# Optimization experiments

Measured on AMD Instinct MI355X. Metric: run time of the kernel, lower is better.

The kernel has to match this reference:

```python
import jax, jax.numpy as jnp
import numpy as np

EMBED_DIM = 1024
NUM_HEADS = 16
HEAD_DIM = EMBED_DIM // NUM_HEADS
SCALE = HEAD_DIM ** -0.5


def setup_inputs() -> dict:
    key = jax.random.key(0)
    ks = jax.random.split(key, 11)
    b, n, c = 2, 2048, EMBED_DIM
    # xavier_uniform bound for square [c, c] weight
    bound = float(np.sqrt(6.0 / (c + c)))
    def xavier(k):
        return jax.random.uniform(k, (c, c), jnp.float32, -bound, bound)
    return {
        "q": jax.random.normal(ks[0], (b, n, c), jnp.float32),
        "k": jax.random.normal(ks[1], (b, n, c), jnp.float32),
        "v": jax.random.normal(ks[2], (b, n, c), jnp.float32),
        "wq": xavier(ks[3]), "bq": jnp.zeros((c,), jnp.float32),
        "wk": xavier(ks[4]), "bk": jnp.zeros((c,), jnp.float32),
        "wv": xavier(ks[5]), "bv": jnp.zeros((c,), jnp.float32),
        "wo": xavier(ks[6]), "bo": jnp.zeros((c,), jnp.float32),
    }


def reference(q, k, v, wq, bq, wk, bk, wv, bv, wo, bo):
    b, n, c = q.shape
    h, d = NUM_HEADS, HEAD_DIM
    # linear projections (torch Linear: x @ W^T + b)
    qh = (q @ wq.T + bq).reshape(b, n, h, d).transpose(0, 2, 1, 3)  # b h n d
    kh = (k @ wk.T + bk).reshape(b, n, h, d).transpose(0, 2, 1, 3)
    vh = (v @ wv.T + bv).reshape(b, n, h, d).transpose(0, 2, 1, 3)
    dots = jnp.einsum('bhid,bhjd->bhij', qh, kh) * SCALE
    attn = jax.nn.softmax(dots, axis=-1)  # dropout p=0 -> identity
    out = jnp.einsum('bhij,bhjd->bhid', attn, vh)
    out = out.transpose(0, 2, 1, 3).reshape(b, n, c)
    return out @ wo.T + bo
```

## Files before the change

kernel.cpp:

```cpp
#include <hip/hip_runtime.h>


typedef float f32x4 __attribute__((ext_vector_type(4)));
typedef float f32x16 __attribute__((ext_vector_type(16)));
typedef __bf16 bf16x8 __attribute__((ext_vector_type(8)));

#define SEQ 2048
#define CH 1024
#define NH 16
#define HD 64
#define TOK 4096
#define QSCALE 0.18033688011112042f

__device__ __forceinline__ unsigned short f2b(float f) {
  unsigned int u = __float_as_uint(f);
  u = (u + 0x7FFFu + ((u >> 16) & 1u)) >> 16;
  return (unsigned short)u;
}

__device__ __forceinline__ float fexp2(float x) {
  float r;
  asm("v_exp_f32 %0, %1" : "=v"(r) : "v"(x));
  return r;
}

__device__ __forceinline__ unsigned int cvtpk(float lo, float hi) {
  unsigned int r;
  asm("v_cvt_pk_bf16_f32 %0, %1, %2" : "=v"(r) : "v"(lo), "v"(hi));
  return r;
}

__device__ __forceinline__ void gload16(const void* g, void* l) {
  __builtin_amdgcn_global_load_lds(
      (const __attribute__((address_space(1))) unsigned int*)g,
      (__attribute__((address_space(3))) unsigned int*)l, 16, 0, 0);
}

struct CvtArgs {
  const float* src[4];
  unsigned short* dst[4];
  int n4[4];
};

__global__ __launch_bounds__(256) void cvt_kernel(CvtArgs a) {
  const int s = blockIdx.y;
  const int n4 = a.n4[s];
  const float4* __restrict__ src = (const float4*)a.src[s];
  unsigned short* __restrict__ dst = a.dst[s];
  const int stride = gridDim.x * blockDim.x;
  for (int i = blockIdx.x * blockDim.x + threadIdx.x; i < n4; i += stride) {
    float4 w = src[i];
    ushort4 o;
    o.x = f2b(w.x); o.y = f2b(w.y); o.z = f2b(w.z); o.w = f2b(w.w);
    *(ushort4*)(dst + 4 * (size_t)i) = o;
  }
}

struct Proj3Args {
  const float* X[3];
  const unsigned short* W[3];
  const float* bias[3];
  unsigned short* outb[3];
  int mode[3];
};

#define P3_ABYTES 16384
#define P3_BUFB (P3_ABYTES + 8192)

__device__ __forceinline__ void p3_stage(
    const float* __restrict__ X, const unsigned short* __restrict__ W,
    int mt, int nt, int k0, unsigned char* buf, int wid, int lane) {
#pragma unroll
  for (int is = 0; is < 4; ++is) {
    const int p = wid * 4096 + is * 1024 + lane * 16;
    const int row = p >> 7;
    const int so = ((p & 127) ^ ((row & 7) << 4)) >> 2;
    gload16(X + (size_t)(mt * 128 + row) * CH + k0 + so, buf + p);
  }
#pragma unroll
  for (int is = 0; is < 2; ++is) {
    const int p = wid * 2048 + is * 1024 + lane * 16;
    const int row = p >> 6;
    const int so = ((p & 63) ^ ((row & 3) << 4)) >> 1;
    gload16(W + (size_t)(nt * 128 + row) * CH + k0 + so, buf + P3_ABYTES + p);
  }
}

__global__ __launch_bounds__(256, 3) void proj3_kernel(Proj3Args a) {
  __shared__ __align__(16) unsigned char smem[2 * P3_BUFB];
  const int z = blockIdx.z;
  const float* __restrict__ X = a.X[z];
  const unsigned short* __restrict__ W = a.W[z];
  const float* __restrict__ bias = a.bias[z];
  unsigned short* __restrict__ outb = a.outb[z];
  const int mode = a.mode[z];
  const int tid = threadIdx.x, wid = tid >> 6, lane = tid & 63;
  const int wm = wid >> 1, wn = wid & 1;
  const int mt = blockIdx.x, nt = blockIdx.y;
  const int l15 = lane & 15, l4 = lane >> 4;

  float bvv[4];
#pragma unroll
  for (int nj = 0; nj < 4; ++nj)
    bvv[nj] = bias[nt * 128 + wn * 64 + nj * 16 + l15];

  f32x4 acc[4][4] = {};

  p3_stage(X, W, mt, nt, 0, smem, wid, lane);
  p3_stage(X, W, mt, nt, 32, smem + P3_BUFB, wid, lane);

  for (int s = 0; s < 32; ++s) {
    if (s < 31) asm volatile("s_waitcnt vmcnt(6)" ::: "memory");
    else        asm volatile("s_waitcnt vmcnt(0)" ::: "memory");
    __builtin_amdgcn_s_barrier();
    __builtin_amdgcn_sched_barrier(0);

    unsigned char* Al = smem + (s & 1) * P3_BUFB;
    unsigned char* Bl = Al + P3_ABYTES;

    bf16x8 af[4], bfr[4];
#pragma unroll
    for (int mi = 0; mi < 4; ++mi) {
      const int r = wm * 64 + mi * 16 + l15;
      const int swz = (r & 7) << 4;
      const f32x4 lo = *(const f32x4*)(Al + r * 128 + ((l4 * 32) ^ swz));
      const f32x4 hi = *(const f32x4*)(Al + r * 128 + ((l4 * 32 + 16) ^ swz));
      const uint4 aw = make_uint4(cvtpk(lo[0], lo[1]), cvtpk(lo[2], lo[3]),
                                  cvtpk(hi[0], hi[1]), cvtpk(hi[2], hi[3]));
      af[mi] = *(const bf16x8*)&aw;
    }
#pragma unroll
    for (int nj = 0; nj < 4; ++nj) {
      const int rb = wn * 64 + nj * 16 + l15;
      bfr[nj] = *(const bf16x8*)(Bl + rb * 64 + ((l4 * 16) ^ ((rb & 3) << 4)));
    }
    __builtin_amdgcn_s_setprio(1);
#pragma unroll
    for (int mi = 0; mi < 4; ++mi)
#pragma unroll
      for (int nj = 0; nj < 4; ++nj)
        acc[mi][nj] = __builtin_amdgcn_mfma_f32_16x16x32_bf16(af[mi], bfr[nj], acc[mi][nj], 0, 0, 0);
    __builtin_amdgcn_s_setprio(0);

    __builtin_amdgcn_s_barrier();
    if (s + 2 < 32)
      p3_stage(X, W, mt, nt, (s + 2) * 32, Al, wid, lane);
  }

  const int row0 = mt * 128 + wm * 64;
  const int col0 = nt * 128 + wn * 64;
#pragma unroll
  for (int nj = 0; nj < 4; ++nj) {
    const int col = col0 + nj * 16 + l15;
    const float bv = bvv[nj];
    const int h = col >> 6, d = col & 63;
    if (mode == 3) {
#pragma unroll
      for (int mi = 0; mi < 4; ++mi) {
        const int row = row0 + mi * 16 + l4 * 4;
        const int b = row >> 11, n = row & (SEQ - 1);
        ushort4 o;
        o.x = f2b(acc[mi][nj][0] + bv);
        o.y = f2b(acc[mi][nj][1] + bv);
        o.z = f2b(acc[mi][nj][2] + bv);
        o.w = f2b(acc[mi][nj][3] + bv);
        *(ushort4*)(outb + ((size_t)(b * NH + h) * HD + d) * SEQ + n) = o;
      }
    } else {
#pragma unroll
      for (int mi = 0; mi < 4; ++mi) {
#pragma unroll
        for (int r = 0; r < 4; ++r) {
          const int row = row0 + mi * 16 + l4 * 4 + r;
          float v = acc[mi][nj][r] + bv;
          if (mode == 0) v *= QSCALE;
          const int b = row >> 11, n = row & (SEQ - 1);
          outb[(((size_t)(b * NH + h) * SEQ + n) << 6) + d] = f2b(v);
        }
      }
    }
  }
}

__device__ __forceinline__ void projo_stage(
    const unsigned short* __restrict__ X, const unsigned short* __restrict__ W,
    int mt, int nt, int k0, unsigned char* buf, int wid, int lane) {
#pragma unroll
  for (int is = 0; is < 2; ++is) {
    const int p = (wid * 2 + is) * 1024 + lane * 16;
    gload16(X + (size_t)(mt * 128 + (p >> 6)) * CH + k0 + ((p & 63) >> 1),
            buf + (wid * 2 + is) * 1024);
  }
  {
    const int p = wid * 1024 + lane * 16;
    gload16(W + (size_t)(nt * 64 + (p >> 6)) * CH + k0 + ((p & 63) >> 1),
            buf + 8192 + wid * 1024);
  }
}

__global__ __launch_bounds__(256, 4) void projo_kernel(
    const unsigned short* __restrict__ X, const unsigned short* __restrict__ W,
    const float* __restrict__ bias, float* __restrict__ outf) {
  constexpr int BUFB = 8192 + 4096;
  __shared__ __align__(16) unsigned char smem[3 * BUFB];
  const int tid = threadIdx.x, wid = tid >> 6, lane = tid & 63;
  const int wm = wid >> 1, wn = wid & 1;
  const int mt = blockIdx.x, nt = blockIdx.y;
  const int l15 = lane & 15, l4 = lane >> 4;

  float bvv[2];
#pragma unroll
  for (int nj = 0; nj < 2; ++nj)
    bvv[nj] = bias[nt * 64 + wn * 32 + nj * 16 + l15];

  f32x4 acc[4][2] = {};

  projo_stage(X, W, mt, nt, 0, smem, wid, lane);
  projo_stage(X, W, mt, nt, 32, smem + BUFB, wid, lane);

  for (int s = 0; s < 32; ++s) {
    if (s < 31) asm volatile("s_waitcnt vmcnt(3)" ::: "memory");
    else        asm volatile("s_waitcnt vmcnt(0)" ::: "memory");
    __builtin_amdgcn_s_barrier();
    __builtin_amdgcn_sched_barrier(0);
    if (s + 2 < 32)
      projo_stage(X, W, mt, nt, (s + 2) * 32, smem + ((s + 2) % 3) * BUFB, wid, lane);

    unsigned char* Al = smem + (s % 3) * BUFB;
    unsigned char* Bl = Al + 8192;
    bf16x8 af[4], bfr[2];
#pragma unroll
    for (int mi = 0; mi < 4; ++mi)
      af[mi] = *(const bf16x8*)(Al + (wm * 64 + mi * 16 + l15) * 64 + l4 * 16);
#pragma unroll
    for (int nj = 0; nj < 2; ++nj)
      bfr[nj] = *(const bf16x8*)(Bl + (wn * 32 + nj * 16 + l15) * 64 + l4 * 16);
    __builtin_amdgcn_s_setprio(1);
#pragma unroll
    for (int mi = 0; mi < 4; ++mi)
#pragma unroll
      for (int nj = 0; nj < 2; ++nj)
        acc[mi][nj] = __builtin_amdgcn_mfma_f32_16x16x32_bf16(af[mi], bfr[nj], acc[mi][nj], 0, 0, 0);
    __builtin_amdgcn_s_setprio(0);
  }

  const int row0 = mt * 128 + wm * 64;
  const int col0 = nt * 64 + wn * 32;
#pragma unroll
  for (int nj = 0; nj < 2; ++nj) {
    const int col = col0 + nj * 16 + l15;
    const float bv = bvv[nj];
#pragma unroll
    for (int mi = 0; mi < 4; ++mi)
#pragma unroll
      for (int r = 0; r < 4; ++r)
        outf[(size_t)(row0 + mi * 16 + l4 * 4 + r) * CH + col] = acc[mi][nj][r] + bv;
  }
}

__device__ __forceinline__ void stage_kv(
    const unsigned short* __restrict__ Kb, const unsigned short* __restrict__ Vb,
    int j0, unsigned char* buf, int ws3, int lane) {
#pragma unroll
  for (int is = 0; is < 2; ++is) {
    const int p = ws3 * 2048 + is * 1024 + lane * 16;
    const int row = p >> 7;
    const int sw = ((p & 127) ^ ((row & 7) << 4)) >> 1;
    gload16(Kb + (size_t)(j0 + row) * HD + sw, buf + ws3 * 2048 + is * 1024);
    gload16(Vb + (size_t)row * SEQ + j0 + sw, buf + 8192 + ws3 * 2048 + is * 1024);
  }
}

__global__ __launch_bounds__(512, 4) void attn_kernel(
    const unsigned short* __restrict__ Qh, const unsigned short* __restrict__ Kh,
    const unsigned short* __restrict__ Vt, unsigned short* __restrict__ AO) {
  __shared__ __align__(16) unsigned char smem[81920];
  const int tid = threadIdx.x, wid = tid >> 6, lane = tid & 63;
  const int l31 = lane & 31, h = lane >> 5;
  const int grp = wid >> 2, wq = wid & 3;
  const int bid = blockIdx.x;
  const int swz = (bid & 7) * 64 + (bid >> 3);
  const int qt = swz & 15, bh = swz >> 4;

  const unsigned short* Qb = Qh + ((size_t)bh * SEQ + qt * 128) * HD;
  const unsigned short* Kb = Kh + (size_t)bh * SEQ * HD;
  const unsigned short* Vb = Vt + (size_t)bh * HD * SEQ;
  unsigned char* kvb = smem + grp * 32768;
  unsigned char* Qreg = smem + 65536;
  const int jbase = grp * 16;

#pragma unroll
  for (int is = 0; is < 4; ++is) {
    const int p = wq * 4096 + is * 1024 + lane * 16;
    const int row = p >> 7;
    const int sw = ((p & 127) ^ ((row & 7) << 4)) >> 1;
    gload16(Qb + (size_t)row * HD + sw, Qreg + wq * 4096 + is * 1024);
  }
  stage_kv(Kb, Vb, jbase * 64, kvb, wq, lane);
  asm volatile("s_waitcnt vmcnt(4)" ::: "memory");

  bf16x8 qf[4];
  const int qrow = wq * 32 + l31;
#pragma unroll
  for (int ks = 0; ks < 4; ++ks)
    qf[ks] = *(const bf16x8*)(Qreg + qrow * 128 +
                              ((ks * 32 + h * 16) ^ ((qrow & 7) << 4)));

  stage_kv(Kb, Vb, (jbase + 1) * 64, kvb + 16384, wq, lane);

  f32x16 O[2] = {};
  float m = -1e30f, l = 0.f;

  for (int it = 0; it < 16; ++it) {
    if (it < 15) asm volatile("s_waitcnt vmcnt(4)" ::: "memory");
    else         asm volatile("s_waitcnt vmcnt(0)" ::: "memory");
    __builtin_amdgcn_s_barrier();
    __builtin_amdgcn_sched_barrier(0);

    unsigned char* Kc = kvb + ((it & 1) << 14);
    unsigned char* Vc = Kc + 8192;

    f32x16 st[2] = {};
    __builtin_amdgcn_s_setprio(1);
#pragma unroll
    for (int kb = 0; kb < 2; ++kb) {
#pragma unroll
      for (int ks = 0; ks < 4; ++ks) {
        const int krow = kb * 32 + l31;
        const bf16x8 kf = *(const bf16x8*)(Kc + krow * 128 +
                                           ((ks * 32 + h * 16) ^ ((krow & 7) << 4)));
        st[kb] = __builtin_amdgcn_mfma_f32_32x32x16_bf16(kf, qf[ks], st[kb], 0, 0, 0);
      }
    }
    __builtin_amdgcn_s_setprio(0);

    float t[8];
#pragma unroll
    for (int i = 0; i < 8; ++i)
      t[i] = fmaxf(fmaxf(st[0][i], st[0][i + 8]), fmaxf(st[1][i], st[1][i + 8]));
#pragma unroll
    for (int i = 0; i < 4; ++i) t[i] = fmaxf(t[i], t[i + 4]);
    float pmax = fmaxf(fmaxf(t[0], t[1]), fmaxf(t[2], t[3]));
    pmax = fmaxf(pmax, __shfl_xor(pmax, 32));
    if (__any(pmax > m + 8.f)) {
      const float mnew = fmaxf(m, pmax);
      const float alpha = fexp2(m - mnew);
#pragma unroll
      for (int r = 0; r < 16; ++r) {
        const int qO = (r & 3) + 8 * (r >> 2) + 4 * h;
        const float aO = __shfl(alpha, qO);
        O[0][r] *= aO;
        O[1][r] *= aO;
      }
      l *= alpha;
      m = mnew;
    }
#pragma unroll
    for (int kb = 0; kb < 2; ++kb)
#pragma unroll
      for (int i = 0; i < 16; ++i) st[kb][i] = fexp2(st[kb][i] - m);
    float s[8];
#pragma unroll
    for (int i = 0; i < 8; ++i)
      s[i] = (st[0][i] + st[0][i + 8]) + (st[1][i] + st[1][i + 8]);
#pragma unroll
    for (int i = 0; i < 4; ++i) s[i] += s[i + 4];
    float rs = (s[0] + s[1]) + (s[2] + s[3]);
    rs += __shfl_xor(rs, 32);
    l += rs;

    unsigned int pk[2][8];
#pragma unroll
    for (int kb = 0; kb < 2; ++kb)
#pragma unroll
      for (int j = 0; j < 8; ++j)
        pk[kb][j] = cvtpk(st[kb][2 * j], st[kb][2 * j + 1]);

    __builtin_amdgcn_s_setprio(1);
#pragma unroll
    for (int kk = 0; kk < 4; ++kk) {
      const int kb = kk >> 1, j0 = (kk & 1) * 4;
      const unsigned int p0 = pk[kb][j0 + 0], p1 = pk[kb][j0 + 1];
      const unsigned int p2 = pk[kb][j0 + 2], p3 = pk[kb][j0 + 3];
      const unsigned int u0 = h ? p0 : p2;
      const unsigned int u1 = h ? p1 : p3;
      const unsigned int su0 = __shfl_xor(u0, 32);
      const unsigned int su1 = __shfl_xor(u1, 32);
      const unsigned int d0 = h ? su0 : p0;
      const unsigned int d1 = h ? su1 : p1;
      const unsigned int d2 = h ? p2 : su0;
      const unsigned int d3 = h ? p3 : su1;
      uint4 aw = make_uint4(d0, d1, d2, d3);
      const bf16x8 af = *(const bf16x8*)&aw;
#pragma unroll
      for (int db = 0; db < 2; ++db) {
        const int vrow = db * 32 + l31;
        const bf16x8 vf = *(const bf16x8*)(Vc + vrow * 128 +
                                           ((kk * 32 + h * 16) ^ ((vrow & 7) << 4)));
        O[db] = __builtin_amdgcn_mfma_f32_32x32x16_bf16(af, vf, O[db], 0, 0, 0);
      }
    }
    __builtin_amdgcn_s_setprio(0);

    __builtin_amdgcn_s_barrier();
    if (it + 2 < 16)
      stage_kv(Kb, Vb, (jbase + it + 2) * 64, Kc, wq, lane);
  }

  float2* slotO = (float2*)(smem + wq * 8960);
  float2* slotML = (float2*)(smem + wq * 8960 + 8704);
  if (grp == 1) {
    float2* dst = slotO + lane * 17;
#pragma unroll
    for (int i = 0; i < 8; ++i) dst[i] = make_float2(O[0][2 * i], O[0][2 * i + 1]);
#pragma unroll
    for (int i = 0; i < 8; ++i) dst[8 + i] = make_float2(O[1][2 * i], O[1][2 * i + 1]);
    if (h == 0) slotML[l31] = make_float2(m, l);
  }
  __builtin_amdgcn_s_barrier();
  if (grp == 0) {
    const float* src = (const float*)(slotO + lane * 17);
    const float2 ml1 = slotML[l31];
    const float mm = fmaxf(m, ml1.x);
    const float a0 = fexp2(m - mm), a1 = fexp2(ml1.x - mm);
    const float inv = 1.f / (a0 * l + a1 * ml1.y);
    const float w0 = a0 * inv, w1 = a1 * inv;
    const int b = bh >> 4, hh = bh & 15;
#pragma unroll
    for (int r = 0; r < 16; ++r) {
      const int qO = (r & 3) + 8 * (r >> 2) + 4 * h;
      const float s0 = __shfl(w0, qO), s1 = __shfl(w1, qO);
      const int n = qt * 128 + wq * 32 + qO;
      const size_t base = ((size_t)(b * SEQ + n)) * CH + hh * HD;
      AO[base + l31] = f2b(O[0][r] * s0 + src[r] * s1);
      AO[base + 32 + l31] = f2b(O[1][r] * s0 + src[16 + r] * s1);
    }
  }
}

extern "C" void kernel_launch(void* const* d_in, const int* in_sizes, int n_in,
                              void* d_out, int out_size, void* d_ws, size_t ws_size,
                              hipStream_t stream) {
  (void)in_sizes; (void)n_in; (void)out_size; (void)ws_size;
  const float* q  = (const float*)d_in[0];
  const float* k  = (const float*)d_in[1];
  const float* v  = (const float*)d_in[2];
  const float* wq = (const float*)d_in[3];
  const float* bq = (const float*)d_in[4];
  const float* wk = (const float*)d_in[5];
  const float* bk = (const float*)d_in[6];
  const float* wv = (const float*)d_in[7];
  const float* bv = (const float*)d_in[8];
  const float* wo = (const float*)d_in[9];
  const float* bo = (const float*)d_in[10];

  unsigned char* ws = (unsigned char*)d_ws;
  const size_t MB8 = 8u << 20;
  unsigned short* AO  = (unsigned short*)(ws + 0 * MB8);
  unsigned short* Vt  = (unsigned short*)(ws + 1 * MB8);
  unsigned short* wqb = (unsigned short*)(ws + 3 * MB8);
  unsigned short* wkb = (unsigned short*)(ws + 3 * MB8 + 1 * 2097152);
  unsigned short* wvb = (unsigned short*)(ws + 3 * MB8 + 2 * 2097152);
  unsigned short* wob = (unsigned short*)(ws + 3 * MB8 + 3 * 2097152);
  unsigned short* Qh  = (unsigned short*)(ws + 4 * MB8);
  unsigned short* Kh  = (unsigned short*)(ws + 5 * MB8);
  float* out = (float*)d_out;

  CvtArgs ca;
  ca.src[0] = wq; ca.dst[0] = wqb; ca.n4[0] = CH * CH / 4;
  ca.src[1] = wk; ca.dst[1] = wkb; ca.n4[1] = CH * CH / 4;
  ca.src[2] = wv; ca.dst[2] = wvb; ca.n4[2] = CH * CH / 4;
  ca.src[3] = wo; ca.dst[3] = wob; ca.n4[3] = CH * CH / 4;
  cvt_kernel<<<dim3(512, 4), 256, 0, stream>>>(ca);

  Proj3Args p3;
  p3.X[0] = q; p3.W[0] = wqb; p3.bias[0] = bq; p3.outb[0] = Qh; p3.mode[0] = 0;
  p3.X[1] = k; p3.W[1] = wkb; p3.bias[1] = bk; p3.outb[1] = Kh; p3.mode[1] = 1;
  p3.X[2] = v; p3.W[2] = wvb; p3.bias[2] = bv; p3.outb[2] = Vt; p3.mode[2] = 3;
  proj3_kernel<<<dim3(32, 8, 3), 256, 0, stream>>>(p3);

  attn_kernel<<<dim3(512), 512, 0, stream>>>(Qh, Kh, Vt, AO);

  projo_kernel<<<dim3(32, 16), 256, 0, stream>>>(AO, wob, bo, out);
}
```

Before: 120.3 us.

## Pre-convert QKV activations to bf16 and simplify projection staging

Extends the conversion kernel to also convert the q, k, v activations to bf16 in a separate pass. The QKV projection kernel then loads bf16 directly, dropping in-loop fp32-to-bf16 conversion, halving LDS per stage and raising the occupancy hint. The swizzled LDS layout is removed, and workspace buffers are reshuffled so Vt lives in the output buffer. This adds an extra full read and write of the activations, and the unswizzled LDS reads may incur bank conflicts.

```diff
diff --git a/kernel.cpp b/kernel.cpp
--- a/kernel.cpp
+++ b/kernel.cpp
@@ -37,9 +37,9 @@
 }
 
 struct CvtArgs {
-  const float* src[4];
-  unsigned short* dst[4];
-  int n4[4];
+  const float* src[7];
+  unsigned short* dst[7];
+  int n4[7];
 };
 
 __global__ __launch_bounds__(256) void cvt_kernel(CvtArgs a) {
@@ -56,40 +56,32 @@
   }
 }
 
-struct Proj3Args {
-  const float* X[3];
+struct ProjQKVArgs {
+  const unsigned short* X[3];
   const unsigned short* W[3];
   const float* bias[3];
   unsigned short* outb[3];
   int mode[3];
 };
 
-#define P3_ABYTES 16384
-#define P3_BUFB (P3_ABYTES + 8192)
-
-__device__ __forceinline__ void p3_stage(
-    const float* __restrict__ X, const unsigned short* __restrict__ W,
+__device__ __forceinline__ void qkv_stage(
+    const unsigned short* __restrict__ X, const unsigned short* __restrict__ W,
     int mt, int nt, int k0, unsigned char* buf, int wid, int lane) {
 #pragma unroll
-  for (int is = 0; is < 4; ++is) {
-    const int p = wid * 4096 + is * 1024 + lane * 16;
-    const int row = p >> 7;
-    const int so = ((p & 127) ^ ((row & 7) << 4)) >> 2;
-    gload16(X + (size_t)(mt * 128 + row) * CH + k0 + so, buf + p);
-  }
-#pragma unroll
   for (int is = 0; is < 2; ++is) {
-    const int p = wid * 2048 + is * 1024 + lane * 16;
+    const int p = (wid * 2 + is) * 1024 + lane * 16;
     const int row = p >> 6;
-    const int so = ((p & 63) ^ ((row & 3) << 4)) >> 1;
-    gload16(W + (size_t)(nt * 128 + row) * CH + k0 + so, buf + P3_ABYTES + p);
-  }
-}
-
-__global__ __launch_bounds__(256, 3) void proj3_kernel(Proj3Args a) {
-  __shared__ __align__(16) unsigned char smem[2 * P3_BUFB];
+    const int ce = (p & 63) >> 1;
+    gload16(X + (size_t)(mt * 128 + row) * CH + k0 + ce, buf + p);
+    gload16(W + (size_t)(nt * 128 + row) * CH + k0 + ce, buf + 8192 + p);
+  }
+}
+
+__global__ __launch_bounds__(256, 4) void projqkv_kernel(ProjQKVArgs a) {
+  constexpr int BUFB = 16384;
+  __shared__ __align__(16) unsigned char smem[2 * BUFB];
   const int z = blockIdx.z;
-  const float* __restrict__ X = a.X[z];
+  const unsigned short* __restrict__ X = a.X[z];
   const unsigned short* __restrict__ W = a.W[z];
   const float* __restrict__ bias = a.bias[z];
   unsigned short* __restrict__ outb = a.outb[z];
@@ -106,34 +98,25 @@
 
   f32x4 acc[4][4] = {};
 
-  p3_stage(X, W, mt, nt, 0, smem, wid, lane);
-  p3_stage(X, W, mt, nt, 32, smem + P3_BUFB, wid, lane);
+  qkv_stage(X, W, mt, nt, 0, smem, wid, lane);
+  qkv_stage(X, W, mt, nt, 32, smem + BUFB, wid, lane);
 
   for (int s = 0; s < 32; ++s) {
-    if (s < 31) asm volatile("s_waitcnt vmcnt(6)" ::: "memory");
+    if (s < 31) asm volatile("s_waitcnt vmcnt(4)" ::: "memory");
     else        asm volatile("s_waitcnt vmcnt(0)" ::: "memory");
     __builtin_amdgcn_s_barrier();
     __builtin_amdgcn_sched_barrier(0);
 
-    unsigned char* Al = smem + (s & 1) * P3_BUFB;
-    unsigned char* Bl = Al + P3_ABYTES;
+    unsigned char* Al = smem + (s & 1) * BUFB;
+    unsigned char* Bl = Al + 8192;
 
     bf16x8 af[4], bfr[4];
 #pragma unroll
-    for (int mi = 0; mi < 4; ++mi) {
-      const int r = wm * 64 + mi * 16 + l15;
-      const int swz = (r & 7) << 4;
-      const f32x4 lo = *(const f32x4*)(Al + r * 128 + ((l4 * 32) ^ swz));
-      const f32x4 hi = *(const f32x4*)(Al + r * 128 + ((l4 * 32 + 16) ^ swz));
-      const uint4 aw = make_uint4(cvtpk(lo[0], lo[1]), cvtpk(lo[2], lo[3]),
-                                  cvtpk(hi[0], hi[1]), cvtpk(hi[2], hi[3]));
-      af[mi] = *(const bf16x8*)&aw;
-    }
-#pragma unroll
-    for (int nj = 0; nj < 4; ++nj) {
-      const int rb = wn * 64 + nj * 16 + l15;
-      bfr[nj] = *(const bf16x8*)(Bl + rb * 64 + ((l4 * 16) ^ ((rb & 3) << 4)));
-    }
+    for (int mi = 0; mi < 4; ++mi)
+      af[mi] = *(const bf16x8*)(Al + (wm * 64 + mi * 16 + l15) * 64 + l4 * 16);
+#pragma unroll
+    for (int nj = 0; nj < 4; ++nj)
+      bfr[nj] = *(const bf16x8*)(Bl + (wn * 64 + nj * 16 + l15) * 64 + l4 * 16);
     __builtin_amdgcn_s_setprio(1);
 #pragma unroll
     for (int mi = 0; mi < 4; ++mi)
@@ -144,7 +127,7 @@
 
     __builtin_amdgcn_s_barrier();
     if (s + 2 < 32)
-      p3_stage(X, W, mt, nt, (s + 2) * 32, Al, wid, lane);
+      qkv_stage(X, W, mt, nt, (s + 2) * 32, Al, wid, lane);
   }
 
   const int row0 = mt * 128 + wm * 64;
@@ -456,28 +439,34 @@
 
   unsigned char* ws = (unsigned char*)d_ws;
   const size_t MB8 = 8u << 20;
-  unsigned short* AO  = (unsigned short*)(ws + 0 * MB8);
-  unsigned short* Vt  = (unsigned short*)(ws + 1 * MB8);
+  unsigned short* qb  = (unsigned short*)(ws + 0 * MB8);
+  unsigned short* kb  = (unsigned short*)(ws + 1 * MB8);
+  unsigned short* vb  = (unsigned short*)(ws + 2 * MB8);
   unsigned short* wqb = (unsigned short*)(ws + 3 * MB8);
   unsigned short* wkb = (unsigned short*)(ws + 3 * MB8 + 1 * 2097152);
   unsigned short* wvb = (unsigned short*)(ws + 3 * MB8 + 2 * 2097152);
   unsigned short* wob = (unsigned short*)(ws + 3 * MB8 + 3 * 2097152);
   unsigned short* Qh  = (unsigned short*)(ws + 4 * MB8);
   unsigned short* Kh  = (unsigned short*)(ws + 5 * MB8);
+  unsigned short* Vt  = (unsigned short*)d_out;
+  unsigned short* AO  = qb;
   float* out = (float*)d_out;
 
   CvtArgs ca;
-  ca.src[0] = wq; ca.dst[0] = wqb; ca.n4[0] = CH * CH / 4;
-  ca.src[1] = wk; ca.dst[1] = wkb; ca.n4[1] = CH * CH / 4;
-  ca.src[2] = wv; ca.dst[2] = wvb; ca.n4[2] = CH * CH / 4;
-  ca.src[3] = wo; ca.dst[3] = wob; ca.n4[3] = CH * CH / 4;
-  cvt_kernel<<<dim3(512, 4), 256, 0, stream>>>(ca);
-
-  Proj3Args p3;
-  p3.X[0] = q; p3.W[0] = wqb; p3.bias[0] = bq; p3.outb[0] = Qh; p3.mode[0] = 0;
-  p3.X[1] = k; p3.W[1] = wkb; p3.bias[1] = bk; p3.outb[1] = Kh; p3.mode[1] = 1;
-  p3.X[2] = v; p3.W[2] = wvb; p3.bias[2] = bv; p3.outb[2] = Vt; p3.mode[2] = 3;
-  proj3_kernel<<<dim3(32, 8, 3), 256, 0, stream>>>(p3);
+  ca.src[0] = q;  ca.dst[0] = qb;  ca.n4[0] = TOK * CH / 4;
+  ca.src[1] = k;  ca.dst[1] = kb;  ca.n4[1] = TOK * CH / 4;
+  ca.src[2] = v;  ca.dst[2] = vb;  ca.n4[2] = TOK * CH / 4;
+  ca.src[3] = wq; ca.dst[3] = wqb; ca.n4[3] = CH * CH / 4;
+  ca.src[4] = wk; ca.dst[4] = wkb; ca.n4[4] = CH * CH / 4;
+  ca.src[5] = wv; ca.dst[5] = wvb; ca.n4[5] = CH * CH / 4;
+  ca.src[6] = wo; ca.dst[6] = wob; ca.n4[6] = CH * CH / 4;
+  cvt_kernel<<<dim3(1024, 7), 256, 0, stream>>>(ca);
+
+  ProjQKVArgs p3;
+  p3.X[0] = qb; p3.W[0] = wqb; p3.bias[0] = bq; p3.outb[0] = Qh; p3.mode[0] = 0;
+  p3.X[1] = kb; p3.W[1] = wkb; p3.bias[1] = bk; p3.outb[1] = Kh; p3.mode[1] = 1;
+  p3.X[2] = vb; p3.W[2] = wvb; p3.bias[2] = bv; p3.outb[2] = Vt; p3.mode[2] = 3;
+  projqkv_kernel<<<dim3(32, 8, 3), 256, 0, stream>>>(p3);
 
   attn_kernel<<<dim3(512), 512, 0, stream>>>(Qh, Kh, Vt, AO);
 
```

Measured after the change: 121.6 us. About the same (+1.1%).
